# Performance work log

Measured on AMD Instinct MI355X. Metric: run time of the kernel, lower is better.

Reference implementation:

```python
import jax, jax.numpy as jnp
import numpy as np

N = 100_000  # nodes
E = 1_200_000  # edges (avg degree 12)
EPS = 1e-5


def setup_inputs() -> dict:
    key = jax.random.key(0)
    ks = jax.random.split(key, 12)

    def w(k, shape):
        fan_in = shape[0]
        return jax.random.normal(k, shape, dtype=jnp.float32) * (1.0 / np.sqrt(fan_in))

    return {
        "x": jax.random.normal(ks[0], (N, 4), dtype=jnp.float32),
        "edge_index": jax.random.randint(ks[1], (2, E), 0, N, dtype=jnp.int32),
        "W1": w(ks[2], (4, 16)), "b1": jnp.zeros(16, jnp.float32),
        "g1": jnp.ones(16, jnp.float32), "bt1": jnp.zeros(16, jnp.float32),
        "W2": w(ks[3], (16, 32)), "b2": jnp.zeros(32, jnp.float32),
        "g2": jnp.ones(32, jnp.float32), "bt2": jnp.zeros(32, jnp.float32),
        "W3": w(ks[4], (32, 64)), "b3": jnp.zeros(64, jnp.float32),
        "g3": jnp.ones(64, jnp.float32), "bt3": jnp.zeros(64, jnp.float32),
        "Wf1": w(ks[5], (64, 32)), "bf1": jnp.zeros(32, jnp.float32),
        "Wf2": w(ks[6], (32, 16)), "bf2": jnp.zeros(16, jnp.float32),
        "Wf3": w(ks[7], (16, 2)), "bf3": jnp.zeros(2, jnp.float32),
    }


def _gcn_conv(x, W, b, src, dst):
    """PyG GCNConv: self-loops + symmetric deg^-1/2 normalization + scatter-add."""
    n = x.shape[0]
    h = x @ W  # [N, out]
    loop = jnp.arange(n, dtype=src.dtype)
    s = jnp.concatenate([src, loop])  # [E+N]
    d = jnp.concatenate([dst, loop])
    deg = jax.ops.segment_sum(jnp.ones_like(d, dtype=h.dtype), d, num_segments=n)
    dinv = jnp.where(deg > 0, jax.lax.rsqrt(deg), 0.0)
    norm = dinv[s] * dinv[d]  # [E+N]
    out = jax.ops.segment_sum(h[s] * norm[:, None], d, num_segments=n)
    return out + b


def _bn(x, g, bt):
    # BatchNorm1d over node dim (batch statistics, training-mode semantics)
    m = jnp.mean(x, axis=0)
    v = jnp.var(x, axis=0)
    return (x - m) * jax.lax.rsqrt(v + EPS) * g + bt


def reference(x, edge_index, W1, b1, g1, bt1, W2, b2, g2, bt2, W3, b3, g3, bt3,
              Wf1, bf1, Wf2, bf2, Wf3, bf3):
    src, dst = edge_index[0], edge_index[1]
    h = jax.nn.elu(_bn(jax.nn.relu(_gcn_conv(x, W1, b1, src, dst)), g1, bt1))
    h = jax.nn.elu(_bn(jax.nn.relu(_gcn_conv(h, W2, b2, src, dst)), g2, bt2))
    h = jax.nn.elu(_bn(jax.nn.relu(_gcn_conv(h, W3, b3, src, dst)), g3, bt3))
    h = jax.nn.elu(h @ Wf1 + bf1)
    h = jax.nn.elu(h @ Wf2 + bf2)
    h = h @ Wf3 + bf3
    return jax.nn.log_softmax(h, axis=1)
```

## Files before the change

### kernel.cpp

```cpp
#include <hip/hip_runtime.h>
#include <hip/hip_fp16.h>
#include <math.h>

#define BN_EPS 1e-5f

union H8 {
  float4 f4;
  __half2 h2[4];
};


#define NHB 512

__global__ void hist_kernel(const int* __restrict__ dst, int* __restrict__ histpart, int e) {
  __shared__ int h[512];
  for (int i = threadIdx.x; i < 512; i += 256) h[i] = 0;
  __syncthreads();
  int stride = gridDim.x * 256;
  for (int i = blockIdx.x * 256 + threadIdx.x; i < e; i += stride)
    atomicAdd(&h[dst[i] >> 8], 1);
  __syncthreads();
  for (int i = threadIdx.x; i < 512; i += 256)
    histpart[blockIdx.x * 512 + i] = h[i];
}

__global__ void scan_buckets(const int* __restrict__ histpart,
                             int* __restrict__ boffset, int* __restrict__ bcursor,
                             int* __restrict__ row_start, int nbuck, int n, int e) {
  __shared__ int sc[512];
  int tid = threadIdx.x;
  int v = 0;
  for (int r = 0; r < NHB; r++) v += histpart[r * 512 + tid];
  sc[tid] = v;
  __syncthreads();
  for (int off = 1; off < 512; off <<= 1) {
    int add = (tid >= off) ? sc[tid - off] : 0;
    __syncthreads();
    sc[tid] += add;
    __syncthreads();
  }
  int excl = sc[tid] - v;
  if (tid <= nbuck) {
    int val = (tid < nbuck) ? excl : e;
    boffset[tid] = val;
    bcursor[tid] = val;
  }
  if (tid == 0) row_start[n] = e;
}

__global__ void partition_kernel(const int* __restrict__ src, const int* __restrict__ dst,
                                 int* __restrict__ bcursor, int* __restrict__ ebuf, int e) {
  __shared__ int h[512];
  __shared__ int base[512];
  const int BLK_E = 4096;
  int e0 = blockIdx.x * BLK_E;
  int e1 = min(e0 + BLK_E, e);
  for (int i = threadIdx.x; i < 512; i += 256) h[i] = 0;
  __syncthreads();
  for (int i = e0 + threadIdx.x; i < e1; i += 256)
    atomicAdd(&h[dst[i] >> 8], 1);
  __syncthreads();
  for (int i = threadIdx.x; i < 512; i += 256) {
    int c = h[i];
    base[i] = (c > 0) ? atomicAdd(&bcursor[i], c) : 0;
    h[i] = 0;
  }
  __syncthreads();
  for (int i = e0 + threadIdx.x; i < e1; i += 256) {
    int d = dst[i];
    int b = d >> 8;
    int r = atomicAdd(&h[b], 1);
    ebuf[base[b] + r] = (src[i] << 8) | (d & 255);
  }
}

__global__ void bucket_fill(const int* __restrict__ ebuf, const int* __restrict__ boffset,
                            const float* __restrict__ x, const float* __restrict__ W1,
                            int* __restrict__ row_start, float* __restrict__ dinv,
                            int* __restrict__ csr_src, float4* __restrict__ hh1, int n) {
  __shared__ int lcnt[256];
  __shared__ int lpre[256];
  __shared__ float w1s[64];
  int bid = blockIdx.x;
  int nb0 = bid << 8;
  int tid = threadIdx.x;
  int e0 = boffset[bid], e1 = boffset[bid + 1];
  lcnt[tid] = 0;
  if (tid < 64) w1s[tid] = W1[tid];
  __syncthreads();
  for (int j = e0 + tid; j < e1; j += 256)
    atomicAdd(&lcnt[ebuf[j] & 255], 1);
  __syncthreads();
  int v = lcnt[tid];
  lpre[tid] = v;
  __syncthreads();
  for (int off = 1; off < 256; off <<= 1) {
    int add = (tid >= off) ? lpre[tid - off] : 0;
    __syncthreads();
    lpre[tid] += add;
    __syncthreads();
  }
  int excl = lpre[tid] - v;
  int node = nb0 + tid;
  if (node < n) {
    row_start[node] = e0 + excl;
    float dnv = rsqrtf((float)(v + 1));
    dinv[node] = dnv;
    float4 xr = ((const float4*)x)[node];
    float acc[16];
#pragma unroll
    for (int c = 0; c < 16; c++)
      acc[c] = xr.x * w1s[c] + xr.y * w1s[16 + c] + xr.z * w1s[32 + c] + xr.w * w1s[48 + c];
    H8 o0, o1;
#pragma unroll
    for (int q = 0; q < 4; q++) {
      o0.h2[q] = __float22half2_rn(make_float2(acc[2 * q] * dnv, acc[2 * q + 1] * dnv));
      o1.h2[q] = __float22half2_rn(make_float2(acc[8 + 2 * q] * dnv, acc[8 + 2 * q + 1] * dnv));
    }
    hh1[(size_t)node * 2] = o0.f4;
    hh1[(size_t)node * 2 + 1] = o1.f4;
  }
  __syncthreads();
  lpre[tid] = excl;
  __syncthreads();
  for (int j = e0 + tid; j < e1; j += 256) {
    int ed = ebuf[j];
    int p = atomicAdd(&lpre[ed & 255], 1);
    csr_src[e0 + p] = ed >> 8;
  }
}

template <int K, int C>
__global__ __launch_bounds__(256) void mm_dinv_h(
    const float4* __restrict__ Xh, const float* __restrict__ stats,
    const float* __restrict__ g, const float* __restrict__ bt,
    const float* __restrict__ W, const float* __restrict__ dinv,
    float4* __restrict__ hh, int n) {
  constexpr int GP8 = C / 8;
  constexpr int KG8 = K / 8;
  __shared__ float w[K * C];
  __shared__ float bsc[K], bsh[K];
  for (int i = threadIdx.x; i < K * C; i += 256) w[i] = W[i];
  if (threadIdx.x < K) {
    int c = threadIdx.x;
    float inv_n = 1.0f / (float)n;
    float m = stats[c] * inv_n;
    float var = fmaxf(stats[K + c] * inv_n - m * m, 0.f);
    float sc = rsqrtf(var + BN_EPS) * g[c];
    bsc[c] = sc;
    bsh[c] = bt[c] - m * sc;
  }
  __syncthreads();

  int idx = blockIdx.x * 256 + threadIdx.x;
  if (idx >= n * GP8) return;
  int nn = idx / GP8;
  int c8 = idx % GP8;

  float acc[8];
#pragma unroll
  for (int t = 0; t < 8; t++) acc[t] = 0.f;

  const float4* rowh = Xh + (size_t)nn * KG8;
#pragma unroll
  for (int j8 = 0; j8 < KG8; j8++) {
    H8 u;
    u.f4 = rowh[j8];
#pragma unroll
    for (int q = 0; q < 4; q++) {
      float2 f = __half22float2(u.h2[q]);
      int k0 = j8 * 8 + 2 * q, k1 = k0 + 1;
      float v0 = f.x * bsc[k0] + bsh[k0];
      v0 = v0 > 0.f ? v0 : (__expf(v0) - 1.f);
      float v1 = f.y * bsc[k1] + bsh[k1];
      v1 = v1 > 0.f ? v1 : (__expf(v1) - 1.f);
      int wb0 = k0 * C + c8 * 8, wb1 = k1 * C + c8 * 8;
#pragma unroll
      for (int t = 0; t < 8; t++) acc[t] += v0 * w[wb0 + t] + v1 * w[wb1 + t];
    }
  }
  float dn = dinv[nn];
  H8 o;
#pragma unroll
  for (int q = 0; q < 4; q++)
    o.h2[q] = __float22half2_rn(make_float2(acc[2 * q] * dn, acc[2 * q + 1] * dn));
  hh[idx] = o.f4;
}

template <int C, int LOGGP>
__global__ __launch_bounds__(256) void gather_finalize_h(
    const float4* __restrict__ hh8, const int* __restrict__ row_start,
    const int* __restrict__ csr_src, const float* __restrict__ dinv,
    const float* __restrict__ bias, float4* __restrict__ act4,
    float* __restrict__ partials, int n) {
  constexpr int GP = C / 8;
  constexpr int NPB = 256 / GP;
  int tid = threadIdx.x;
  int c8 = tid & (GP - 1);
  int local = tid >> LOGGP;
  int n0 = blockIdx.x * NPB + local;
  bool valid = (n0 < n);

  float vo[8];
#pragma unroll
  for (int t = 0; t < 8; t++) vo[t] = 0.f;

  if (valid) {
    float acc[8];
    {
      H8 u;
      u.f4 = hh8[(size_t)n0 * GP + c8];
#pragma unroll
      for (int q = 0; q < 4; q++) {
        float2 f = __half22float2(u.h2[q]);
        acc[2 * q] = f.x;
        acc[2 * q + 1] = f.y;
      }
    }
    int s = row_start[n0], e0 = row_start[n0 + 1];
    int j = s;
    for (; j + 8 <= e0; j += 8) {
      H8 u[8];
#pragma unroll
      for (int m = 0; m < 8; m++) u[m].f4 = hh8[(size_t)csr_src[j + m] * GP + c8];
#pragma unroll
      for (int m = 0; m < 8; m++)
#pragma unroll
        for (int q = 0; q < 4; q++) {
          float2 f = __half22float2(u[m].h2[q]);
          acc[2 * q] += f.x;
          acc[2 * q + 1] += f.y;
        }
    }
    for (; j + 4 <= e0; j += 4) {
      H8 u[4];
#pragma unroll
      for (int m = 0; m < 4; m++) u[m].f4 = hh8[(size_t)csr_src[j + m] * GP + c8];
#pragma unroll
      for (int m = 0; m < 4; m++)
#pragma unroll
        for (int q = 0; q < 4; q++) {
          float2 f = __half22float2(u[m].h2[q]);
          acc[2 * q] += f.x;
          acc[2 * q + 1] += f.y;
        }
    }
    for (; j < e0; j++) {
      H8 u;
      u.f4 = hh8[(size_t)csr_src[j] * GP + c8];
#pragma unroll
      for (int q = 0; q < 4; q++) {
        float2 f = __half22float2(u.h2[q]);
        acc[2 * q] += f.x;
        acc[2 * q + 1] += f.y;
      }
    }

    float dn = dinv[n0];
    const float4* bias4 = (const float4*)bias;
    float4 blo = bias4[c8 * 2], bhi = bias4[c8 * 2 + 1];
    vo[0] = fmaxf(dn * acc[0] + blo.x, 0.f);
    vo[1] = fmaxf(dn * acc[1] + blo.y, 0.f);
    vo[2] = fmaxf(dn * acc[2] + blo.z, 0.f);
    vo[3] = fmaxf(dn * acc[3] + blo.w, 0.f);
    vo[4] = fmaxf(dn * acc[4] + bhi.x, 0.f);
    vo[5] = fmaxf(dn * acc[5] + bhi.y, 0.f);
    vo[6] = fmaxf(dn * acc[6] + bhi.z, 0.f);
    vo[7] = fmaxf(dn * acc[7] + bhi.w, 0.f);
    H8 o;
#pragma unroll
    for (int q = 0; q < 4; q++)
      o.h2[q] = __float22half2_rn(make_float2(vo[2 * q], vo[2 * q + 1]));
    act4[(size_t)n0 * GP + c8] = o.f4;
  }

  __shared__ float redS[8 * 256];
  __shared__ float redQ[8 * 256];
#pragma unroll
  for (int t = 0; t < 8; t++) {
    redS[t * 256 + tid] = vo[t];
    redQ[t * 256 + tid] = vo[t] * vo[t];
  }
#pragma unroll
  for (int off = NPB / 2; off >= 1; off >>= 1) {
    __syncthreads();
    if (local < off) {
#pragma unroll
      for (int t = 0; t < 8; t++) {
        redS[t * 256 + tid] += redS[t * 256 + tid + off * GP];
        redQ[t * 256 + tid] += redQ[t * 256 + tid + off * GP];
      }
    }
  }
  __syncthreads();
  if (local == 0) {
#pragma unroll
    for (int t = 0; t < 8; t++) {
      partials[(size_t)blockIdx.x * 2 * C + c8 * 8 + t] = redS[t * 256 + tid];
      partials[(size_t)blockIdx.x * 2 * C + C + c8 * 8 + t] = redQ[t * 256 + tid];
    }
  }
}

template <int C2>
__global__ void reduce_partials(const float* __restrict__ partials,
                                float* __restrict__ stats, int rows) {
  int ch = blockIdx.x;
  float acc = 0.f;
  for (int r = threadIdx.x; r < rows; r += 256)
    acc += partials[(size_t)r * C2 + ch];
  __shared__ float red[256];
  red[threadIdx.x] = acc;
  __syncthreads();
#pragma unroll
  for (int off = 128; off >= 1; off >>= 1) {
    if (threadIdx.x < off) red[threadIdx.x] += red[threadIdx.x + off];
    __syncthreads();
  }
  if (threadIdx.x == 0) stats[ch] = red[0];
}


__global__ __launch_bounds__(256) void head_kernel(
    const float4* __restrict__ h16,
    const float* __restrict__ st3, const float* __restrict__ g3,
    const float* __restrict__ bt3,
    const float* __restrict__ Wf1, const float* __restrict__ bf1,
    const float* __restrict__ Wf2, const float* __restrict__ bf2,
    const float* __restrict__ Wf3, const float* __restrict__ bf3,
    float* __restrict__ out, int n) {
  __shared__ float w1[64 * 32], w2[32 * 16], w3[32];
  __shared__ float sb1[32], sb2[16], sb3[2];
  __shared__ float bsc[64], bsh[64];
  __shared__ float a1s[32][128];
  __shared__ float a2s[16][128];
  int tid = threadIdx.x;
  for (int i = tid; i < 64 * 32; i += 256) w1[i] = Wf1[i];
  for (int i = tid; i < 32 * 16; i += 256) w2[i] = Wf2[i];
  if (tid < 64) {
    float inv_n = 1.0f / (float)n;
    float m = st3[tid] * inv_n;
    float var = fmaxf(st3[64 + tid] * inv_n - m * m, 0.f);
    float sc = rsqrtf(var + BN_EPS) * g3[tid];
    bsc[tid] = sc;
    bsh[tid] = bt3[tid] - m * sc;
  }
  if (tid < 32) {
    w3[tid] = Wf3[tid];
    sb1[tid] = bf1[tid];
  }
  if (tid < 16) sb2[tid] = bf2[tid];
  if (tid < 2) sb3[tid] = bf3[tid];
  __syncthreads();

  int node = tid & 127;
  int half = tid >> 7;
  int n0 = blockIdx.x * 128 + node;
  bool valid = (n0 < n);

  float a1[16];
#pragma unroll
  for (int c = 0; c < 16; c++) a1[c] = sb1[half * 16 + c];
  if (valid) {
    const float4* hrow = h16 + (size_t)n0 * 8;
#pragma unroll
    for (int j = 0; j < 8; j++) {
      H8 u;
      u.f4 = hrow[j];
#pragma unroll
      for (int q = 0; q < 4; q++) {
        float2 f = __half22float2(u.h2[q]);
        int k0 = j * 8 + 2 * q, k1 = k0 + 1;
        float v0 = f.x * bsc[k0] + bsh[k0];
        v0 = v0 > 0.f ? v0 : (__expf(v0) - 1.f);
        float v1 = f.y * bsc[k1] + bsh[k1];
        v1 = v1 > 0.f ? v1 : (__expf(v1) - 1.f);
#pragma unroll
        for (int c = 0; c < 16; c++)
          a1[c] += v0 * w1[k0 * 32 + half * 16 + c] + v1 * w1[k1 * 32 + half * 16 + c];
      }
    }
  }
#pragma unroll
  for (int c = 0; c < 16; c++) {
    float v = a1[c];
    a1s[half * 16 + c][node] = v > 0.f ? v : (__expf(v) - 1.f);
  }
  __syncthreads();

  float a2[8];
#pragma unroll
  for (int c = 0; c < 8; c++) a2[c] = sb2[half * 8 + c];
#pragma unroll
  for (int k = 0; k < 32; k++) {
    float ak = a1s[k][node];
#pragma unroll
    for (int c = 0; c < 8; c++) a2[c] += ak * w2[k * 16 + half * 8 + c];
  }
#pragma unroll
  for (int c = 0; c < 8; c++) {
    float v = a2[c];
    a2s[half * 8 + c][node] = v > 0.f ? v : (__expf(v) - 1.f);
  }
  __syncthreads();

  if (half == 0 && valid) {
    float z0 = sb3[0], z1 = sb3[1];
#pragma unroll
    for (int k = 0; k < 16; k++) {
      float ak = a2s[k][node];
      z0 += ak * w3[k * 2 + 0];
      z1 += ak * w3[k * 2 + 1];
    }
    float mx = fmaxf(z0, z1);
    float lse = mx + __logf(__expf(z0 - mx) + __expf(z1 - mx));
    out[(size_t)n0 * 2 + 0] = z0 - lse;
    out[(size_t)n0 * 2 + 1] = z1 - lse;
  }
}


extern "C" void kernel_launch(void* const* d_in, const int* in_sizes, int n_in,
                              void* d_out, int out_size, void* d_ws, size_t ws_size,
                              hipStream_t stream) {
  const float* x = (const float*)d_in[0];
  const int* ei = (const int*)d_in[1];
  const float* W1 = (const float*)d_in[2];  const float* b1 = (const float*)d_in[3];
  const float* g1 = (const float*)d_in[4];  const float* bt1 = (const float*)d_in[5];
  const float* W2 = (const float*)d_in[6];  const float* b2 = (const float*)d_in[7];
  const float* g2 = (const float*)d_in[8];  const float* bt2 = (const float*)d_in[9];
  const float* W3 = (const float*)d_in[10]; const float* b3 = (const float*)d_in[11];
  const float* g3 = (const float*)d_in[12]; const float* bt3 = (const float*)d_in[13];
  const float* Wf1 = (const float*)d_in[14]; const float* bf1 = (const float*)d_in[15];
  const float* Wf2 = (const float*)d_in[16]; const float* bf2 = (const float*)d_in[17];
  const float* Wf3 = (const float*)d_in[18]; const float* bf3 = (const float*)d_in[19];
  float* out = (float*)d_out;

  const int N = in_sizes[0] / 4;
  const int E = in_sizes[1] / 2;
  const int* srcp = ei;
  const int* dstp = ei + E;
  const int NBUCK = (N + 255) >> 8;

  char* ws = (char*)d_ws;
  size_t off = 0;
  auto alloc = [&](size_t bytes) {
    off = (off + 255) & ~(size_t)255;
    size_t o = off;
    off += bytes;
    return o;
  };
  float* dinv      = (float*)(ws + alloc((size_t)N * 4));
  int*   row_start = (int*)  (ws + alloc((size_t)(N + 1) * 4));
  int*   histpart  = (int*)  (ws + alloc((size_t)NHB * 512 * 4));
  float* stats     = (float*)(ws + alloc((size_t)224 * 4));
  int*   boffset   = (int*)  (ws + alloc((size_t)513 * 4));
  int*   bcursor   = (int*)  (ws + alloc((size_t)513 * 4));
  int*   csr_src   = (int*)  (ws + alloc((size_t)E * 4));
  float* partials  = (float*)(ws + alloc((size_t)3200 * 128 * 4));
  float* bufH      = (float*)(ws + alloc((size_t)N * 64 * 2));
  float* bufAct    = (float*)(ws + alloc((size_t)N * 64 * 2));
  float* st1 = stats;
  float* st2 = stats + 32;
  float* st3 = stats + 96;
  int*   ebuf = (int*)bufAct;

  hist_kernel<<<NHB, 256, 0, stream>>>(dstp, histpart, E);
  scan_buckets<<<1, 512, 0, stream>>>(histpart, boffset, bcursor, row_start, NBUCK, N, E);
  partition_kernel<<<(E + 4095) / 4096, 256, 0, stream>>>(srcp, dstp, bcursor, ebuf, E);
  bucket_fill<<<NBUCK, 256, 0, stream>>>(ebuf, boffset, x, W1, row_start, dinv, csr_src,
                                         (float4*)bufH, N);

  int g1n = (N + 127) / 128;
  gather_finalize_h<16, 1><<<g1n, 256, 0, stream>>>(
      (const float4*)bufH, row_start, csr_src, dinv, b1, (float4*)bufAct, partials, N);
  reduce_partials<32><<<32, 256, 0, stream>>>(partials, st1, g1n);

  int g2n = (N + 63) / 64;
  mm_dinv_h<16, 32><<<(N * 4 + 255) / 256, 256, 0, stream>>>(
      (const float4*)bufAct, st1, g1, bt1, W2, dinv, (float4*)bufH, N);
  gather_finalize_h<32, 2><<<g2n, 256, 0, stream>>>(
      (const float4*)bufH, row_start, csr_src, dinv, b2, (float4*)bufAct, partials, N);
  reduce_partials<64><<<64, 256, 0, stream>>>(partials, st2, g2n);

  int g3n = (N + 31) / 32;
  mm_dinv_h<32, 64><<<(N * 8 + 255) / 256, 256, 0, stream>>>(
      (const float4*)bufAct, st2, g2, bt2, W3, dinv, (float4*)bufH, N);
  gather_finalize_h<64, 3><<<g3n, 256, 0, stream>>>(
      (const float4*)bufH, row_start, csr_src, dinv, b3, (float4*)bufAct, partials, N);
  reduce_partials<128><<<128, 256, 0, stream>>>(partials, st3, g3n);

  head_kernel<<<(N + 127) / 128, 256, 0, stream>>>(
      (const float4*)bufAct, st3, g3, bt3, Wf1, bf1, Wf2, bf2, Wf3, bf3, out, N);
}
```

Before: 201.4 us.

## Fuse BN stat reduction into gather via slotted atomics and last-block finalize

Removes the three reduce_partials launches. Each gather block now atomically adds its per-channel sums into one of 32 slot rows, and the last block to finish (found with a global counter and a threadfence) sums the slots into the stats. Slots and counters are zeroed inside scan_buckets. The histogram grid also drops from 512 to 128 blocks, which shortens the scan's serial loop. The cost is atomic contention and a last-block reduction, and float atomics make the sums order-dependent so results are not bitwise deterministic.

Measured after the change: 575.1 us. 186% more time.

```diff
diff --git a/kernel.cpp b/kernel.cpp
--- a/kernel.cpp
+++ b/kernel.cpp
@@ -10,7 +10,7 @@
 };
 
 
-#define NHB 512
+#define NHB 128
 
 __global__ void hist_kernel(const int* __restrict__ dst, int* __restrict__ histpart, int e) {
   __shared__ int h[512];
@@ -26,9 +26,12 @@
 
 __global__ void scan_buckets(const int* __restrict__ histpart,
                              int* __restrict__ boffset, int* __restrict__ bcursor,
-                             int* __restrict__ row_start, int nbuck, int n, int e) {
+                             int* __restrict__ row_start, float* __restrict__ slotbuf,
+                             int* __restrict__ counters, int nbuck, int n, int e) {
   __shared__ int sc[512];
   int tid = threadIdx.x;
+  for (int i = tid; i < 3 * 32 * 128; i += 512) slotbuf[i] = 0.f;
+  if (tid < 3) counters[tid] = 0;
   int v = 0;
   for (int r = 0; r < NHB; r++) v += histpart[r * 512 + tid];
   sc[tid] = v;
@@ -192,7 +195,8 @@
     const float4* __restrict__ hh8, const int* __restrict__ row_start,
     const int* __restrict__ csr_src, const float* __restrict__ dinv,
     const float* __restrict__ bias, float4* __restrict__ act4,
-    float* __restrict__ partials, int n) {
+    float* __restrict__ slots, int* __restrict__ counter,
+    float* __restrict__ stats, int n) {
   constexpr int GP = C / 8;
   constexpr int NPB = 256 / GP;
   int tid = threadIdx.x;
@@ -293,31 +297,32 @@
     }
   }
   __syncthreads();
-  if (local == 0) {
+  if (tid < GP) {
+    int sb = (blockIdx.x & 31) * 128;
 #pragma unroll
     for (int t = 0; t < 8; t++) {
-      partials[(size_t)blockIdx.x * 2 * C + c8 * 8 + t] = redS[t * 256 + tid];
-      partials[(size_t)blockIdx.x * 2 * C + C + c8 * 8 + t] = redQ[t * 256 + tid];
-    }
-  }
-}
-
-template <int C2>
-__global__ void reduce_partials(const float* __restrict__ partials,
-                                float* __restrict__ stats, int rows) {
-  int ch = blockIdx.x;
-  float acc = 0.f;
-  for (int r = threadIdx.x; r < rows; r += 256)
-    acc += partials[(size_t)r * C2 + ch];
-  __shared__ float red[256];
-  red[threadIdx.x] = acc;
-  __syncthreads();
-#pragma unroll
-  for (int off = 128; off >= 1; off >>= 1) {
-    if (threadIdx.x < off) red[threadIdx.x] += red[threadIdx.x + off];
-    __syncthreads();
-  }
-  if (threadIdx.x == 0) stats[ch] = red[0];
+      atomicAdd(&slots[sb + c8 * 8 + t], redS[t * 256 + tid]);
+      atomicAdd(&slots[sb + 64 + c8 * 8 + t], redQ[t * 256 + tid]);
+    }
+  }
+
+  __shared__ int isLast;
+  __threadfence();
+  __syncthreads();
+  if (tid == 0) {
+    int old = atomicAdd(counter, 1);
+    isLast = (old == (int)gridDim.x - 1) ? 1 : 0;
+  }
+  __syncthreads();
+  if (isLast && tid < C) {
+    float a = 0.f, b = 0.f;
+    for (int s = 0; s < 32; s++) {
+      a += slots[s * 128 + tid];
+      b += slots[s * 128 + 64 + tid];
+    }
+    stats[tid] = a;
+    stats[C + tid] = b;
+  }
 }
 
 
@@ -454,10 +459,11 @@
   int*   row_start = (int*)  (ws + alloc((size_t)(N + 1) * 4));
   int*   histpart  = (int*)  (ws + alloc((size_t)NHB * 512 * 4));
   float* stats     = (float*)(ws + alloc((size_t)224 * 4));
+  float* slotbuf   = (float*)(ws + alloc((size_t)3 * 32 * 128 * 4));
+  int*   counters  = (int*)  (ws + alloc((size_t)16 * 4));
   int*   boffset   = (int*)  (ws + alloc((size_t)513 * 4));
   int*   bcursor   = (int*)  (ws + alloc((size_t)513 * 4));
   int*   csr_src   = (int*)  (ws + alloc((size_t)E * 4));
-  float* partials  = (float*)(ws + alloc((size_t)3200 * 128 * 4));
   float* bufH      = (float*)(ws + alloc((size_t)N * 64 * 2));
   float* bufAct    = (float*)(ws + alloc((size_t)N * 64 * 2));
   float* st1 = stats;
@@ -466,29 +472,30 @@
   int*   ebuf = (int*)bufAct;
 
   hist_kernel<<<NHB, 256, 0, stream>>>(dstp, histpart, E);
-  scan_buckets<<<1, 512, 0, stream>>>(histpart, boffset, bcursor, row_start, NBUCK, N, E);
+  scan_buckets<<<1, 512, 0, stream>>>(histpart, boffset, bcursor, row_start,
+                                      slotbuf, counters, NBUCK, N, E);
   partition_kernel<<<(E + 4095) / 4096, 256, 0, stream>>>(srcp, dstp, bcursor, ebuf, E);
   bucket_fill<<<NBUCK, 256, 0, stream>>>(ebuf, boffset, x, W1, row_start, dinv, csr_src,
                                          (float4*)bufH, N);
 
   int g1n = (N + 127) / 128;
   gather_finalize_h<16, 1><<<g1n, 256, 0, stream>>>(
-      (const float4*)bufH, row_start, csr_src, dinv, b1, (float4*)bufAct, partials, N);
-  reduce_partials<32><<<32, 256, 0, stream>>>(partials, st1, g1n);
+      (const float4*)bufH, row_start, csr_src, dinv, b1, (float4*)bufAct,
+      slotbuf, counters, st1, N);
 
   int g2n = (N + 63) / 64;
   mm_dinv_h<16, 32><<<(N * 4 + 255) / 256, 256, 0, stream>>>(
       (const float4*)bufAct, st1, g1, bt1, W2, dinv, (float4*)bufH, N);
   gather_finalize_h<32, 2><<<g2n, 256, 0, stream>>>(
-      (const float4*)bufH, row_start, csr_src, dinv, b2, (float4*)bufAct, partials, N);
-  reduce_partials<64><<<64, 256, 0, stream>>>(partials, st2, g2n);
+      (const float4*)bufH, row_start, csr_src, dinv, b2, (float4*)bufAct,
+      slotbuf + 32 * 128, counters + 1, st2, N);
 
   int g3n = (N + 31) / 32;
   mm_dinv_h<32, 64><<<(N * 8 + 255) / 256, 256, 0, stream>>>(
       (const float4*)bufAct, st2, g2, bt2, W3, dinv, (float4*)bufH, N);
   gather_finalize_h<64, 3><<<g3n, 256, 0, stream>>>(
-      (const float4*)bufH, row_start, csr_src, dinv, b3, (float4*)bufAct, partials, N);
-  reduce_partials<128><<<128, 256, 0, stream>>>(partials, st3, g3n);
+      (const float4*)bufH, row_start, csr_src, dinv, b3, (float4*)bufAct,
+      slotbuf + 2 * 32 * 128, counters + 2, st3, N);
 
   head_kernel<<<(N + 127) / 128, 256, 0, stream>>>(
       (const float4*)bufAct, st3, g3, bt3, Wf1, bf1, Wf2, bf2, Wf3, bf3, out, N);
```
